# Optimization experiments

Hardware: AMD Instinct MI355X
Metric: run time of the kernel (lower is better)

Reference implementation:

```python
import jax, jax.numpy as jnp
import numpy as np

NUM_HEADS = 8


def setup_inputs() -> dict:
    key = jax.random.key(0)
    ks = jax.random.split(key, 5)
    B, C, H, W = 2, 256, 64, 64
    # 0.02 scaling keeps logits in a sane range so softmax is not one-hot
    return {
        "x": jax.random.normal(ks[0], (B, C, H, W), dtype=jnp.float32),
        "w_qkv": jax.random.normal(ks[1], (3 * C, C), dtype=jnp.float32) * 0.02,
        "b_qkv": jax.random.normal(ks[2], (3 * C,), dtype=jnp.float32) * 0.02,
        "w_proj": jax.random.normal(ks[3], (C, C), dtype=jnp.float32) * 0.02,
        "b_proj": jax.random.normal(ks[4], (C,), dtype=jnp.float32) * 0.02,
    }


def reference(x, w_qkv, b_qkv, w_proj, b_proj):
    B, C, H, W = x.shape
    N = H * W
    h = NUM_HEADS
    d = C // h
    # 1x1 conv == per-pixel linear: (B,C,H,W) -> (B,3C,H,W)
    qkv = jnp.einsum('oc,bchw->bohw', w_qkv, x) + b_qkv[None, :, None, None]
    qkv = qkv.reshape(B, 3, h, d, N)
    # q,k,v: (B, h, N, d)
    q = jnp.swapaxes(qkv[:, 0], -2, -1)
    k = jnp.swapaxes(qkv[:, 1], -2, -1)
    v = jnp.swapaxes(qkv[:, 2], -2, -1)
    scale = d ** (-0.5)
    attn = jax.nn.softmax(jnp.einsum('bhnd,bhmd->bhnm', q, k) * scale, axis=-1)
    out = jnp.einsum('bhnm,bhmd->bhnd', attn, v)  # (B, h, N, d)
    # faithful to torch: transpose(1,2) -> (B,N,h,d), then row-major reshape to (B,C,H,W)
    out = jnp.swapaxes(out, 1, 2).reshape(B, C, H, W)
    out = jnp.einsum('oc,bchw->bohw', w_proj, out) + b_proj[None, :, None, None]
    return out
```

## Files before the change

kernel.cpp:

```cpp
#include <hip/hip_runtime.h>
#include <hip/hip_bf16.h>


typedef __bf16 bf16;
typedef __bf16 bf16x4 __attribute__((ext_vector_type(4)));
typedef __bf16 bf16x8 __attribute__((ext_vector_type(8)));
typedef float  f32x4  __attribute__((ext_vector_type(4)));
typedef short  s16x4  __attribute__((ext_vector_type(4)));

#if __has_builtin(__builtin_amdgcn_mfma_f32_16x16x16bf16_1k)
#define HAVE_MFMA16 1
#endif

#if __has_builtin(__builtin_amdgcn_exp2f)
#define EXP2(x) __builtin_amdgcn_exp2f(x)
#else
#define EXP2(x) exp2f(x)
#endif

#define NS 4096
#define QSCALE (0.17677669529663687f * 1.4426950408889634f)

static __device__ inline unsigned pack2(float a, float b) {
  union { bf16 h[2]; unsigned u; } v;
  v.h[0] = (bf16)a; v.h[1] = (bf16)b;
  return v.u;
}

__global__ __launch_bounds__(256) void qkv_fused(
    const float* __restrict__ x, const float* __restrict__ w,
    const float* __restrict__ bias,
    bf16* __restrict__ qbuf, bf16* __restrict__ kbuf, bf16* __restrict__ vbuf)
{
  __shared__ bf16 As[64 * 264];
  __shared__ bf16 Bs[64 * 264];
  const int n0 = blockIdx.x * 64, o0 = blockIdx.y * 64, b = blockIdx.z;
  const int t = threadIdx.x;
  const int wv = t >> 6, L = t & 63, quad = L >> 4, lb = L & 15;

  {
    unsigned* A32 = (unsigned*)As;
    const int nj = (t & 15) * 4;
#pragma unroll
    for (int p = 0; p < 8; p++) {
      const int c = p * 32 + (t >> 4) * 2;
      const float* xr = x + ((size_t)(b * 256 + c)) * NS + n0 + nj;
      f32x4 va = *(const f32x4*)xr;
      f32x4 vb = *(const f32x4*)(xr + NS);
#pragma unroll
      for (int i = 0; i < 4; i++)
        A32[(nj + i) * 132 + (c >> 1)] = pack2(va[i], vb[i]);
    }
  }
  {
    const int cj = (t & 15) * 16;
#pragma unroll
    for (int p = 0; p < 4; p++) {
      const int r = p * 16 + (t >> 4);
      const float* wr = w + (size_t)(o0 + r) * 256 + cj;
      f32x4 w0 = *(const f32x4*)wr,       w1 = *(const f32x4*)(wr + 4);
      f32x4 w2 = *(const f32x4*)(wr + 8), w3 = *(const f32x4*)(wr + 12);
      bf16x8 lo, hi;
#pragma unroll
      for (int i = 0; i < 4; i++) {
        lo[i] = (bf16)w0[i]; lo[4 + i] = (bf16)w1[i];
        hi[i] = (bf16)w2[i]; hi[4 + i] = (bf16)w3[i];
      }
      *(bf16x8*)&Bs[r * 264 + cj] = lo;
      *(bf16x8*)&Bs[r * 264 + cj + 8] = hi;
    }
  }
  __syncthreads();

  f32x4 acc[4] = {};
#pragma unroll
  for (int ks = 0; ks < 8; ks++) {
    const bf16x8 bfr = *(const bf16x8*)&Bs[(wv * 16 + lb) * 264 + ks * 32 + quad * 8];
#pragma unroll
    for (int a = 0; a < 4; a++) {
      const bf16x8 afr = *(const bf16x8*)&As[(a * 16 + lb) * 264 + ks * 32 + quad * 8];
      acc[a] = __builtin_amdgcn_mfma_f32_16x16x32_bf16(afr, bfr, acc[a], 0, 0, 0);
    }
  }

  const int comp = o0 >> 8;
  const int o = o0 + wv * 16 + lb;
  const float bv = bias[o];
  if (comp < 2) {
    bf16* dst = (comp == 0) ? qbuf : kbuf;
    const float sc = (comp == 0) ? QSCALE : 1.0f;
    const int hh = (o & 255) >> 5, dd = o & 31;
    const size_t base = ((size_t)b * 8 + hh) * NS;
#pragma unroll
    for (int a = 0; a < 4; a++)
#pragma unroll
      for (int r = 0; r < 4; r++) {
        const int n = n0 + a * 16 + quad * 4 + r;
        dst[(base + n) * 32 + dd] = (bf16)((acc[a][r] + bv) * sc);
      }
  } else {
    __syncthreads();
    bf16* Vt2 = As;
#pragma unroll
    for (int a = 0; a < 4; a++)
#pragma unroll
      for (int r = 0; r < 4; r++)
        Vt2[(wv * 16 + lb) * 72 + a * 16 + quad * 4 + r] = (bf16)(acc[a][r] + bv);
    __syncthreads();
    const int row = t & 63;
    const int o2 = o0 + row;
    const int hh2 = (o2 & 255) >> 5, dd2 = o2 & 31;
    const int hc = (t >> 6) * 16;
    bf16x8 v0 = *(const bf16x8*)&Vt2[row * 72 + hc];
    bf16x8 v1 = *(const bf16x8*)&Vt2[row * 72 + hc + 8];
    bf16* vd = vbuf + (((size_t)b * 8 + hh2) * 32 + dd2) * NS + n0 + hc;
    *(bf16x8*)vd = v0;
    *(bf16x8*)(vd + 8) = v1;
  }
}

#define KS_OFF 0
#define VT_OFF 2560
#define KV_SZ  (2560 + 32 * 72)

__global__ __launch_bounds__(512) void attn_kernel(
    const bf16* __restrict__ qbuf, const bf16* __restrict__ kbuf,
    const bf16* __restrict__ vbuf, bf16* __restrict__ abuf)
{
  __shared__ bf16 KV[2][KV_SZ];
#ifndef HAVE_MFMA16
  __shared__ bf16 Ps[8][16 * 72];
#endif

  const int qb = blockIdx.x;
  const int bh = blockIdx.y;
  const bf16* Q  = qbuf + (size_t)bh * NS * 32;
  const bf16* K  = kbuf + (size_t)bh * NS * 32;
  const bf16* Vt = vbuf + (size_t)bh * 32 * NS;

  const int t = threadIdx.x;
  const int wv = t >> 6, L = t & 63, quad = L >> 4, lb = L & 15;
  const int qrow = qb * 128 + wv * 16;

  const bf16x8 qfrag = *(const bf16x8*)(Q + (size_t)(qrow + lb) * 32 + quad * 8);

  const int u = t & 255;
  const bool kside = t < 256;
  const int soff = kside ? ((u >> 2) * 40 + (u & 3) * 8)
                         : (VT_OFF + (u >> 3) * 72 + (u & 7) * 8);
  const bf16* gsrc = kside ? (K + (size_t)(u >> 2) * 32 + (u & 3) * 8)
                           : (Vt + (size_t)(u >> 3) * NS + (u & 7) * 8);
  const int gstep = kside ? 64 * 32 : 64;

  bf16x8 reg = *(const bf16x8*)gsrc;

  f32x4 oacc0 = {0.f, 0.f, 0.f, 0.f};
  f32x4 oacc1 = {0.f, 0.f, 0.f, 0.f};
  f32x4 oacc2 = {0.f, 0.f, 0.f, 0.f};
  const f32x4 zero4 = {0.f, 0.f, 0.f, 0.f};
#ifdef HAVE_MFMA16
  const s16x4 ones = {(short)0x3F80, (short)0x3F80, (short)0x3F80, (short)0x3F80};
#else
  float l_i = 0.f;
#endif

#pragma unroll 2
  for (int kt = 0; kt < 64; kt++) {
    const int buf = kt & 1;
    *(bf16x8*)&KV[buf][soff] = reg;
    __syncthreads();
    if (kt < 63) reg = *(const bf16x8*)(gsrc + (size_t)(kt + 1) * gstep);

    f32x4 st[4];
#pragma unroll
    for (int bi = 0; bi < 4; bi++) {
      const bf16x8 kf = *(const bf16x8*)&KV[buf][(bi * 16 + lb) * 40 + quad * 8];
      st[bi] = __builtin_amdgcn_mfma_f32_16x16x32_bf16(kf, qfrag, zero4, 0, 0, 0);
    }

#pragma unroll
    for (int bi = 0; bi < 4; bi++)
#pragma unroll
      for (int r = 0; r < 4; r++) st[bi][r] = EXP2(st[bi][r]);

#ifdef HAVE_MFMA16
#pragma unroll
    for (int bi = 0; bi < 4; bi++) {
      bf16x4 pb;
#pragma unroll
      for (int r = 0; r < 4; r++) pb[r] = (bf16)st[bi][r];
      const s16x4 pf = __builtin_bit_cast(s16x4, pb);
      const s16x4 vf0 = __builtin_bit_cast(s16x4,
          *(const bf16x4*)&KV[buf][VT_OFF + lb * 72 + bi * 16 + quad * 4]);
      const s16x4 vf1 = __builtin_bit_cast(s16x4,
          *(const bf16x4*)&KV[buf][VT_OFF + (16 + lb) * 72 + bi * 16 + quad * 4]);
      oacc0 = __builtin_amdgcn_mfma_f32_16x16x16bf16_1k(pf, vf0, oacc0, 0, 0, 0);
      oacc1 = __builtin_amdgcn_mfma_f32_16x16x16bf16_1k(pf, vf1, oacc1, 0, 0, 0);
      oacc2 = __builtin_amdgcn_mfma_f32_16x16x16bf16_1k(pf, ones, oacc2, 0, 0, 0);
    }
#else
    {
      float ls = 0.f;
#pragma unroll
      for (int bi = 0; bi < 4; bi++)
#pragma unroll
        for (int r = 0; r < 4; r++) ls += st[bi][r];
      l_i += ls;
      bf16* P = &Ps[wv][0];
#pragma unroll
      for (int bi = 0; bi < 4; bi++) {
        bf16x4 pk;
#pragma unroll
        for (int r = 0; r < 4; r++) pk[r] = (bf16)st[bi][r];
        *(bf16x4*)&P[lb * 72 + bi * 16 + quad * 4] = pk;
      }
#pragma unroll
      for (int ch = 0; ch < 2; ch++) {
        const bf16x8 pf  = *(const bf16x8*)&P[lb * 72 + ch * 32 + quad * 8];
        const bf16x8 vf0 = *(const bf16x8*)&KV[buf][VT_OFF + lb * 72 + ch * 32 + quad * 8];
        const bf16x8 vf1 = *(const bf16x8*)&KV[buf][VT_OFF + (16 + lb) * 72 + ch * 32 + quad * 8];
        oacc0 = __builtin_amdgcn_mfma_f32_16x16x32_bf16(pf, vf0, oacc0, 0, 0, 0);
        oacc1 = __builtin_amdgcn_mfma_f32_16x16x32_bf16(pf, vf1, oacc1, 0, 0, 0);
      }
    }
#endif
  }

  const int b_ = bh >> 3;
  const int hh = bh & 7;
#ifndef HAVE_MFMA16
  float lf = l_i;
  lf += __shfl_xor(lf, 16);
  lf += __shfl_xor(lf, 32);
#endif
#pragma unroll
  for (int r = 0; r < 4; r++) {
#ifdef HAVE_MFMA16
    const float lr = oacc2[r];
#else
    const float lr = __shfl(lf, (quad << 4) | (quad * 4 + r));
#endif
#if __has_builtin(__builtin_amdgcn_rcpf)
    const float inv = __builtin_amdgcn_rcpf(lr);
#else
    const float inv = 1.0f / lr;
#endif
    const int n = qrow + quad * 4 + r;
    bf16* dst = abuf + ((size_t)b_ * NS + n) * 256 + hh * 32;
    dst[lb]      = (bf16)(oacc0[r] * inv);
    dst[16 + lb] = (bf16)(oacc1[r] * inv);
  }
}

__global__ __launch_bounds__(256) void proj_fused(
    const bf16* __restrict__ abuf, const float* __restrict__ w,
    const float* __restrict__ bias, float* __restrict__ out)
{
  __shared__ bf16 As[64 * 264];
  __shared__ bf16 Bs[64 * 264];
  const int ch0 = blockIdx.x * 64, o0 = blockIdx.y * 64;
  const int z = blockIdx.z, b = z >> 4, sHi = z & 15;
  const int t = threadIdx.x;
  const int wv = t >> 6, L = t & 63, quad = L >> 4, lb = L & 15;

  {
    const int cj = (t & 15) * 16;
#pragma unroll
    for (int p = 0; p < 4; p++) {
      const int r = p * 16 + (t >> 4);
      const float* wr = w + (size_t)(o0 + r) * 256 + cj;
      f32x4 w0 = *(const f32x4*)wr,       w1 = *(const f32x4*)(wr + 4);
      f32x4 w2 = *(const f32x4*)(wr + 8), w3 = *(const f32x4*)(wr + 12);
      bf16x8 lo, hi;
#pragma unroll
      for (int i = 0; i < 4; i++) {
        lo[i] = (bf16)w0[i]; lo[4 + i] = (bf16)w1[i];
        hi[i] = (bf16)w2[i]; hi[4 + i] = (bf16)w3[i];
      }
      *(bf16x8*)&As[r * 264 + cj] = lo;
      *(bf16x8*)&As[r * 264 + cj + 8] = hi;
    }
  }
  {
    const int chj = (t & 7) * 8;
#pragma unroll
    for (int p = 0; p < 8; p++) {
      const int c = p * 32 + (t >> 3);
      bf16x8 v = *(const bf16x8*)(abuf +
          ((size_t)b * NS + (size_t)c * 16 + sHi) * 256 + ch0 + chj);
#pragma unroll
      for (int i = 0; i < 8; i++) Bs[(chj + i) * 264 + c] = v[i];
    }
  }
  __syncthreads();

  f32x4 acc[4] = {};
#pragma unroll
  for (int ks = 0; ks < 8; ks++) {
    const bf16x8 bfr = *(const bf16x8*)&Bs[(wv * 16 + lb) * 264 + ks * 32 + quad * 8];
#pragma unroll
    for (int a = 0; a < 4; a++) {
      const bf16x8 afr = *(const bf16x8*)&As[(a * 16 + lb) * 264 + ks * 32 + quad * 8];
      acc[a] = __builtin_amdgcn_mfma_f32_16x16x32_bf16(afr, bfr, acc[a], 0, 0, 0);
    }
  }

  const int ch = ch0 + wv * 16 + lb;
#pragma unroll
  for (int a = 0; a < 4; a++)
#pragma unroll
    for (int r = 0; r < 4; r++) {
      const int o = o0 + a * 16 + quad * 4 + r;
      out[((size_t)b * 256 + o) * NS + sHi * 256 + ch] = acc[a][r] + bias[o];
    }
}

extern "C" void kernel_launch(void* const* d_in, const int* in_sizes, int n_in,
                              void* d_out, int out_size, void* d_ws, size_t ws_size,
                              hipStream_t stream) {
  const float* x      = (const float*)d_in[0];
  const float* w_qkv  = (const float*)d_in[1];
  const float* b_qkv  = (const float*)d_in[2];
  const float* w_proj = (const float*)d_in[3];
  const float* b_proj = (const float*)d_in[4];
  float* out = (float*)d_out;

  char* ws = (char*)d_ws;
  const size_t MB = 1024 * 1024;
  bf16* qbuf = (bf16*)(ws);
  bf16* kbuf = (bf16*)(ws + 4 * MB);
  bf16* vbuf = (bf16*)(ws + 8 * MB);
  bf16* abuf = (bf16*)(ws + 12 * MB);

  qkv_fused<<<dim3(64, 12, 2), 256, 0, stream>>>(x, w_qkv, b_qkv, qbuf, kbuf, vbuf);
  attn_kernel<<<dim3(32, 16), 512, 0, stream>>>(qbuf, kbuf, vbuf, abuf);
  proj_fused<<<dim3(4, 4, 32), 256, 0, stream>>>(abuf, w_proj, b_proj, out);
}
```

Before: 151.6 us.

## Pre-convert weights to bf16 and restructure QKV GEMM to load x once per block

Adds a small kernel that converts the QKV and projection weights to bf16 once per call, folding the Q scale into the weights. The QKV kernel now takes 32 pixels per block and loops over all 768 output channels, so x is read and converted only once instead of 12 times. Weight fragments are read directly from global memory (L2) rather than staged in LDS. The projection kernel likewise reads pre-converted bf16 weights from global memory. The cost is an extra launch, plus more global weight traffic and lower per-block parallelism in the QKV stage.

```diff
diff --git a/kernel.cpp b/kernel.cpp
--- a/kernel.cpp
+++ b/kernel.cpp
@@ -27,99 +27,113 @@
   return v.u;
 }
 
-__global__ __launch_bounds__(256) void qkv_fused(
-    const float* __restrict__ x, const float* __restrict__ w,
+__global__ __launch_bounds__(256) void wcvt(
+    const float* __restrict__ wq, const float* __restrict__ wp,
+    bf16* __restrict__ wqb, bf16* __restrict__ wpb)
+{
+  const int bid = blockIdx.x, t = threadIdx.x;
+  if (bid < 96) {
+    const int i = (bid * 256 + t) * 8;
+    const float sc = (i < 65536) ? QSCALE : 1.0f;
+    f32x4 a = *(const f32x4*)(wq + i);
+    f32x4 b = *(const f32x4*)(wq + i + 4);
+    bf16x8 o;
+#pragma unroll
+    for (int j = 0; j < 4; j++) { o[j] = (bf16)(a[j] * sc); o[4 + j] = (bf16)(b[j] * sc); }
+    *(bf16x8*)(wqb + i) = o;
+  } else {
+    const int i = ((bid - 96) * 256 + t) * 8;
+    f32x4 a = *(const f32x4*)(wp + i);
+    f32x4 b = *(const f32x4*)(wp + i + 4);
+    bf16x8 o;
+#pragma unroll
+    for (int j = 0; j < 4; j++) { o[j] = (bf16)a[j]; o[4 + j] = (bf16)b[j]; }
+    *(bf16x8*)(wpb + i) = o;
+  }
+}
+
+__global__ __launch_bounds__(512) void qkv_fused(
+    const float* __restrict__ x, const bf16* __restrict__ wqb,
     const float* __restrict__ bias,
     bf16* __restrict__ qbuf, bf16* __restrict__ kbuf, bf16* __restrict__ vbuf)
 {
-  __shared__ bf16 As[64 * 264];
-  __shared__ bf16 Bs[64 * 264];
-  const int n0 = blockIdx.x * 64, o0 = blockIdx.y * 64, b = blockIdx.z;
+  __shared__ bf16 As[32 * 264];
+  __shared__ bf16 Vt2[2][64 * 40];
+  const int n0 = blockIdx.x * 32, b = blockIdx.z ? 1 : blockIdx.y;
+  const int bb = blockIdx.y;
   const int t = threadIdx.x;
   const int wv = t >> 6, L = t & 63, quad = L >> 4, lb = L & 15;
+  const int grp = wv >> 2, g = wv & 3;
+  (void)b;
 
   {
     unsigned* A32 = (unsigned*)As;
-    const int nj = (t & 15) * 4;
-#pragma unroll
-    for (int p = 0; p < 8; p++) {
-      const int c = p * 32 + (t >> 4) * 2;
-      const float* xr = x + ((size_t)(b * 256 + c)) * NS + n0 + nj;
+    const int nj = (t & 7) * 4;
+    const int cpair = t >> 3;
+#pragma unroll
+    for (int pass = 0; pass < 2; pass++) {
+      const int c = pass * 128 + cpair * 2;
+      const float* xr = x + ((size_t)(bb * 256 + c)) * NS + n0 + nj;
       f32x4 va = *(const f32x4*)xr;
       f32x4 vb = *(const f32x4*)(xr + NS);
 #pragma unroll
       for (int i = 0; i < 4; i++)
-        A32[(nj + i) * 132 + (c >> 1)] = pack2(va[i], vb[i]);
-    }
-  }
-  {
-    const int cj = (t & 15) * 16;
-#pragma unroll
-    for (int p = 0; p < 4; p++) {
-      const int r = p * 16 + (t >> 4);
-      const float* wr = w + (size_t)(o0 + r) * 256 + cj;
-      f32x4 w0 = *(const f32x4*)wr,       w1 = *(const f32x4*)(wr + 4);
-      f32x4 w2 = *(const f32x4*)(wr + 8), w3 = *(const f32x4*)(wr + 12);
-      bf16x8 lo, hi;
-#pragma unroll
-      for (int i = 0; i < 4; i++) {
-        lo[i] = (bf16)w0[i]; lo[4 + i] = (bf16)w1[i];
-        hi[i] = (bf16)w2[i]; hi[4 + i] = (bf16)w3[i];
-      }
-      *(bf16x8*)&Bs[r * 264 + cj] = lo;
-      *(bf16x8*)&Bs[r * 264 + cj + 8] = hi;
+        A32[(nj + i) * 132 + pass * 64 + cpair] = pack2(va[i], vb[i]);
     }
   }
   __syncthreads();
 
-  f32x4 acc[4] = {};
-#pragma unroll
-  for (int ks = 0; ks < 8; ks++) {
-    const bf16x8 bfr = *(const bf16x8*)&Bs[(wv * 16 + lb) * 264 + ks * 32 + quad * 8];
-#pragma unroll
-    for (int a = 0; a < 4; a++) {
-      const bf16x8 afr = *(const bf16x8*)&As[(a * 16 + lb) * 264 + ks * 32 + quad * 8];
-      acc[a] = __builtin_amdgcn_mfma_f32_16x16x32_bf16(afr, bfr, acc[a], 0, 0, 0);
-    }
-  }
-
-  const int comp = o0 >> 8;
-  const int o = o0 + wv * 16 + lb;
-  const float bv = bias[o];
-  if (comp < 2) {
-    bf16* dst = (comp == 0) ? qbuf : kbuf;
-    const float sc = (comp == 0) ? QSCALE : 1.0f;
-    const int hh = (o & 255) >> 5, dd = o & 31;
-    const size_t base = ((size_t)b * 8 + hh) * NS;
-#pragma unroll
-    for (int a = 0; a < 4; a++)
-#pragma unroll
-      for (int r = 0; r < 4; r++) {
-        const int n = n0 + a * 16 + quad * 4 + r;
-        dst[(base + n) * 32 + dd] = (bf16)((acc[a][r] + bv) * sc);
-      }
-  } else {
-    __syncthreads();
-    bf16* Vt2 = As;
-#pragma unroll
-    for (int a = 0; a < 4; a++)
-#pragma unroll
-      for (int r = 0; r < 4; r++)
-        Vt2[(wv * 16 + lb) * 72 + a * 16 + quad * 4 + r] = (bf16)(acc[a][r] + bv);
-    __syncthreads();
-    const int row = t & 63;
-    const int o2 = o0 + row;
-    const int hh2 = (o2 & 255) >> 5, dd2 = o2 & 31;
-    const int hc = (t >> 6) * 16;
-    bf16x8 v0 = *(const bf16x8*)&Vt2[row * 72 + hc];
-    bf16x8 v1 = *(const bf16x8*)&Vt2[row * 72 + hc + 8];
-    bf16* vd = vbuf + (((size_t)b * 8 + hh2) * 32 + dd2) * NS + n0 + hc;
-    *(bf16x8*)vd = v0;
-    *(bf16x8*)(vd + 8) = v1;
-  }
-}
-
-#define KS_OFF 0
+#pragma unroll
+  for (int op = 0; op < 6; op++) {
+    const int ot = op * 2 + grp;
+    const int o = ot * 64 + g * 16 + lb;
+    f32x4 acc[2] = {};
+#pragma unroll
+    for (int ks = 0; ks < 8; ks++) {
+      const bf16x8 bfr = *(const bf16x8*)(wqb + (size_t)o * 256 + ks * 32 + quad * 8);
+#pragma unroll
+      for (int a = 0; a < 2; a++) {
+        const bf16x8 afr = *(const bf16x8*)&As[(a * 16 + lb) * 264 + ks * 32 + quad * 8];
+        acc[a] = __builtin_amdgcn_mfma_f32_16x16x32_bf16(afr, bfr, acc[a], 0, 0, 0);
+      }
+    }
+
+    const int comp = ot >> 2;
+    const float bv = bias[o] * (comp == 0 ? QSCALE : 1.0f);
+    if (comp < 2) {
+      bf16* dst = (comp == 0) ? qbuf : kbuf;
+      const int hh = (o & 255) >> 5, dd = o & 31;
+      const size_t base = ((size_t)bb * 8 + hh) * NS;
+#pragma unroll
+      for (int a = 0; a < 2; a++)
+#pragma unroll
+        for (int r = 0; r < 4; r++) {
+          const int n = n0 + a * 16 + quad * 4 + r;
+          dst[(base + n) * 32 + dd] = (bf16)(acc[a][r] + bv);
+        }
+    } else {
+#pragma unroll
+      for (int a = 0; a < 2; a++) {
+        bf16x4 pk;
+#pragma unroll
+        for (int r = 0; r < 4; r++) pk[r] = (bf16)(acc[a][r] + bv);
+        *(bf16x4*)&Vt2[grp][(g * 16 + lb) * 40 + a * 16 + quad * 4] = pk;
+      }
+      __syncthreads();
+      {
+        const int grp2 = t >> 8, u = t & 255;
+        const int row = u >> 2, nc = (u & 3) * 8;
+        const int ot2 = op * 2 + grp2;
+        const int o2 = ot2 * 64 + row;
+        const int hh2 = (o2 & 255) >> 5, dd2 = o2 & 31;
+        bf16x8 v = *(const bf16x8*)&Vt2[grp2][row * 40 + nc];
+        *(bf16x8*)(vbuf + (((size_t)bb * 8 + hh2) * 32 + dd2) * NS + n0 + nc) = v;
+      }
+      __syncthreads();
+    }
+  }
+}
+
 #define VT_OFF 2560
 #define KV_SZ  (2560 + 32 * 72)
 
@@ -253,10 +267,9 @@
 }
 
 __global__ __launch_bounds__(256) void proj_fused(
-    const bf16* __restrict__ abuf, const float* __restrict__ w,
+    const bf16* __restrict__ abuf, const bf16* __restrict__ wpb,
     const float* __restrict__ bias, float* __restrict__ out)
 {
-  __shared__ bf16 As[64 * 264];
   __shared__ bf16 Bs[64 * 264];
   const int ch0 = blockIdx.x * 64, o0 = blockIdx.y * 64;
   const int z = blockIdx.z, b = z >> 4, sHi = z & 15;
@@ -264,24 +277,6 @@
   const int wv = t >> 6, L = t & 63, quad = L >> 4, lb = L & 15;
 
   {
-    const int cj = (t & 15) * 16;
-#pragma unroll
-    for (int p = 0; p < 4; p++) {
-      const int r = p * 16 + (t >> 4);
-      const float* wr = w + (size_t)(o0 + r) * 256 + cj;
-      f32x4 w0 = *(const f32x4*)wr,       w1 = *(const f32x4*)(wr + 4);
-      f32x4 w2 = *(const f32x4*)(wr + 8), w3 = *(const f32x4*)(wr + 12);
-      bf16x8 lo, hi;
-#pragma unroll
-      for (int i = 0; i < 4; i++) {
-        lo[i] = (bf16)w0[i]; lo[4 + i] = (bf16)w1[i];
-        hi[i] = (bf16)w2[i]; hi[4 + i] = (bf16)w3[i];
-      }
-      *(bf16x8*)&As[r * 264 + cj] = lo;
-      *(bf16x8*)&As[r * 264 + cj + 8] = hi;
-    }
-  }
-  {
     const int chj = (t & 7) * 8;
 #pragma unroll
     for (int p = 0; p < 8; p++) {
@@ -300,7 +295,8 @@
     const bf16x8 bfr = *(const bf16x8*)&Bs[(wv * 16 + lb) * 264 + ks * 32 + quad * 8];
 #pragma unroll
     for (int a = 0; a < 4; a++) {
-      const bf16x8 afr = *(const bf16x8*)&As[(a * 16 + lb) * 264 + ks * 32 + quad * 8];
+      const bf16x8 afr = *(const bf16x8*)(wpb +
+          (size_t)(o0 + a * 16 + lb) * 256 + ks * 32 + quad * 8);
       acc[a] = __builtin_amdgcn_mfma_f32_16x16x32_bf16(afr, bfr, acc[a], 0, 0, 0);
     }
   }
@@ -331,8 +327,11 @@
   bf16* kbuf = (bf16*)(ws + 4 * MB);
   bf16* vbuf = (bf16*)(ws + 8 * MB);
   bf16* abuf = (bf16*)(ws + 12 * MB);
-
-  qkv_fused<<<dim3(64, 12, 2), 256, 0, stream>>>(x, w_qkv, b_qkv, qbuf, kbuf, vbuf);
+  bf16* wqb  = (bf16*)(ws + 16 * MB);
+  bf16* wpb  = (bf16*)(ws + 17 * MB);
+
+  wcvt<<<dim3(128), 256, 0, stream>>>(w_qkv, w_proj, wqb, wpb);
+  qkv_fused<<<dim3(128, 2), 512, 0, stream>>>(x, wqb, b_qkv, qbuf, kbuf, vbuf);
   attn_kernel<<<dim3(32, 16), 512, 0, stream>>>(qbuf, kbuf, vbuf, abuf);
-  proj_fused<<<dim3(4, 4, 32), 256, 0, stream>>>(abuf, w_proj, b_proj, out);
-}
+  proj_fused<<<dim3(4, 4, 32), 256, 0, stream>>>(abuf, wpb, b_proj, out);
+}
```

Result: slower. 157.3 us (+3.8%).
